# Kernel optimization log

Measured on AMD Instinct MI355X. Metric: run time of the kernel, lower is better.

Reference implementation:

```python
import jax, jax.numpy as jnp
import numpy as np

N_NODES = 50000
N_EDGES = 600000
F_IN = 128
HID = 128
N_CLASSES = 10


def _gcn_graph(edge_index, n_nodes):
    # PyG GCNConv: add self-loops, deg computed on target (col) with weight 1,
    # norm_e = deg^-1/2[src] * deg^-1/2[dst]
    src = jnp.concatenate([edge_index[0], jnp.arange(n_nodes, dtype=edge_index.dtype)])
    dst = jnp.concatenate([edge_index[1], jnp.arange(n_nodes, dtype=edge_index.dtype)])
    deg = jax.ops.segment_sum(jnp.ones_like(dst, dtype=jnp.float32), dst, num_segments=n_nodes)
    dinv = jnp.where(deg > 0, jax.lax.rsqrt(deg), 0.0)
    norm = dinv[src] * dinv[dst]  # [E+N]
    return src, dst, norm


def _gcn_layer(x, W, b, src, dst, norm, n_nodes):
    h = x @ W                      # [N, out] linear first (bias applied post-agg)
    m = h[src] * norm[:, None]     # gather + scale, [E+N, out]
    out = jax.ops.segment_sum(m, dst, num_segments=n_nodes)  # scatter-add
    return out + b


def setup_inputs() -> dict:
    key = jax.random.key(0)
    ks = jax.random.split(key, 4)
    x = jax.random.normal(ks[0], (N_NODES, F_IN), dtype=jnp.float32)
    edge_index = jax.random.randint(ks[1], (2, N_EDGES), 0, N_NODES, dtype=jnp.int64)
    # Glorot-ish init scale for weights
    W_stack = jax.random.normal(ks[2], (8, HID, HID), dtype=jnp.float32) * (1.0 / np.sqrt(HID))
    b_stack = jnp.zeros((8, HID), dtype=jnp.float32)
    W_out = jax.random.normal(ks[3], (HID, N_CLASSES), dtype=jnp.float32) * (1.0 / np.sqrt(HID))
    b_out = jnp.zeros((N_CLASSES,), dtype=jnp.float32)
    return {"x": x, "edge_index": edge_index, "W_stack": W_stack, "b_stack": b_stack,
            "W_out": W_out, "b_out": b_out}


def reference(x, edge_index, W_stack, b_stack, W_out, b_out):
    n_nodes = x.shape[0]
    src, dst, norm = _gcn_graph(edge_index, n_nodes)
    h = x
    for i in range(8):  # conv1..conv8 with ELU
        h = jax.nn.elu(_gcn_layer(h, W_stack[i], b_stack[i], src, dst, norm, n_nodes))
    # conv9: no activation
    return _gcn_layer(h, W_out, b_out, src, dst, norm, n_nodes)
```

## Files before the change

kernel.cpp:

```cpp
#include <hip/hip_runtime.h>
#include <math.h>

#define NN 50000
#define NE 600000
#define HID 128
#define NCLS 10
#define T2S 16

typedef __bf16 bf16x8 __attribute__((ext_vector_type(8)));
typedef float f32x16 __attribute__((ext_vector_type(16)));

__device__ __forceinline__ void split3(float f, ushort& h, ushort& m, ushort& l) {
    unsigned uh = __float_as_uint(f) & 0xffff0000u;
    float fm = f - __uint_as_float(uh);
    unsigned um = __float_as_uint(fm) & 0xffff0000u;
    float fl = fm - __uint_as_float(um);
    h = (ushort)(uh >> 16);
    m = (ushort)(um >> 16);
    l = (ushort)(__float_as_uint(fl) >> 16);
}


__global__ __launch_bounds__(256) void k_count(const int* __restrict__ edge,
                                               int* __restrict__ counts) {
    int e = blockIdx.x * 256 + threadIdx.x;
    if (e < NE) atomicAdd(&counts[edge[NE + e]], 1);
}

__device__ __forceinline__ int wave_incl_scan(int x, int lane) {
#pragma unroll
    for (int off = 1; off < 64; off <<= 1) {
        int y = __shfl_up(x, off, 64);
        if (lane >= off) x += y;
    }
    return x;
}

__global__ __launch_bounds__(256) void k_scan1(const int* __restrict__ counts,
                                               int* __restrict__ rowptr,
                                               int* __restrict__ bsum,
                                               float* __restrict__ dinv) {
    __shared__ int ws[4];
    int tid = threadIdx.x;
    int i = blockIdx.x * 256 + tid;
    int lane = tid & 63, wv = tid >> 6;
    int v = (i < NN) ? counts[i] : 0;
    if (i < NN) dinv[i] = rsqrtf((float)(v + 1));
    int x = wave_incl_scan(v, lane);
    if (lane == 63) ws[wv] = x;
    __syncthreads();
    int off = 0;
    for (int j = 0; j < wv; ++j) off += ws[j];
    if (i < NN) rowptr[i] = off + x - v;
    if (tid == 255) bsum[blockIdx.x] = off + x;
}

__global__ __launch_bounds__(256) void k_scan2(int* __restrict__ bsum, int n) {
    __shared__ int ws[4];
    int tid = threadIdx.x;
    int lane = tid & 63, wv = tid >> 6;
    int v = (tid < n) ? bsum[tid] : 0;
    int x = wave_incl_scan(v, lane);
    if (lane == 63) ws[wv] = x;
    __syncthreads();
    int off = 0;
    for (int j = 0; j < wv; ++j) off += ws[j];
    __syncthreads();
    if (tid < n) bsum[tid] = off + x - v;
}

__global__ __launch_bounds__(256) void k_scan3(int* __restrict__ rowptr,
                                               const int* __restrict__ bsum) {
    int i = blockIdx.x * 256 + threadIdx.x;
    if (i < NN) rowptr[i] += bsum[blockIdx.x];
    if (i == 0) rowptr[NN] = NE;
}

__global__ __launch_bounds__(256) void k_fill(const int* __restrict__ edge,
                                              const int* __restrict__ rowptr,
                                              int* __restrict__ cursor,
                                              const float* __restrict__ dinv,
                                              int2* __restrict__ csr) {
    int e = blockIdx.x * 256 + threadIdx.x;
    if (e >= NE) return;
    int s = edge[e], d = edge[NE + e];
    int slot = atomicSub(&cursor[d], 1) - 1;
    csr[rowptr[d] + slot] = make_int2(s, __float_as_int(dinv[s] * dinv[d]));
}


__global__ __launch_bounds__(256) void k_split_w(const float* __restrict__ Wst,
                                                 ushort* __restrict__ Wt4) {
    int i = blockIdx.x * 256 + threadIdx.x;
    if (i >= 8 * HID * HID) return;
    int l = i >> 14;
    int k = (i >> 7) & 127;
    int n = i & 127;
    ushort h, m, lo;
    split3(Wst[i], h, m, lo);
    int ks = k >> 4, r = k & 15;
    size_t base = ((((size_t)l * 3) * 8 + ks) * 128 + n) * 16 + r;
    const size_t pstride = (size_t)8 * 128 * 16;
    Wt4[base] = h;
    Wt4[base + pstride] = m;
    Wt4[base + 2 * pstride] = lo;
}


__global__ __launch_bounds__(256) void k_mfma_gemm(const float* __restrict__ H,
                                                   const ushort* __restrict__ Wt,
                                                   float* __restrict__ T) {
    int tid = threadIdx.x;
    int lane = tid & 63, w = tid >> 6;
    int l31 = lane & 31, lh = lane >> 5;
    int rowbase = blockIdx.x * 128;

    int grow = rowbase + w * 32 + l31;
    if (grow >= NN) grow = NN - 1;
    const float* arow = H + (size_t)grow * HID + lh * 8;

    const ushort* wbase = Wt + (size_t)l31 * 16 + lh * 8;

    f32x16 acc[4] = {};

#pragma unroll 2
    for (int s = 0; s < 8; ++s) {
        const float4* ap = (const float4*)(arow + s * 16);
        float4 f0 = ap[0], f1 = ap[1];
        float av[8] = {f0.x, f0.y, f0.z, f0.w, f1.x, f1.y, f1.z, f1.w};
        union { ushort u[8]; bf16x8 v; } ah, am, al;
#pragma unroll
        for (int q = 0; q < 8; ++q) split3(av[q], ah.u[q], am.u[q], al.u[q]);

        uint4 bf[3][4];
#pragma unroll
        for (int p = 0; p < 3; ++p)
#pragma unroll
            for (int c = 0; c < 4; ++c)
                bf[p][c] = *(const uint4*)(wbase + (((size_t)p * 8 + s) * 128 + c * 32) * 16);

#pragma unroll
        for (int c = 0; c < 4; ++c)
            acc[c] = __builtin_amdgcn_mfma_f32_32x32x16_bf16(ah.v, *(const bf16x8*)&bf[0][c], acc[c], 0, 0, 0);
#pragma unroll
        for (int c = 0; c < 4; ++c)
            acc[c] = __builtin_amdgcn_mfma_f32_32x32x16_bf16(ah.v, *(const bf16x8*)&bf[1][c], acc[c], 0, 0, 0);
#pragma unroll
        for (int c = 0; c < 4; ++c)
            acc[c] = __builtin_amdgcn_mfma_f32_32x32x16_bf16(am.v, *(const bf16x8*)&bf[0][c], acc[c], 0, 0, 0);
#pragma unroll
        for (int c = 0; c < 4; ++c)
            acc[c] = __builtin_amdgcn_mfma_f32_32x32x16_bf16(ah.v, *(const bf16x8*)&bf[2][c], acc[c], 0, 0, 0);
#pragma unroll
        for (int c = 0; c < 4; ++c)
            acc[c] = __builtin_amdgcn_mfma_f32_32x32x16_bf16(am.v, *(const bf16x8*)&bf[1][c], acc[c], 0, 0, 0);
#pragma unroll
        for (int c = 0; c < 4; ++c)
            acc[c] = __builtin_amdgcn_mfma_f32_32x32x16_bf16(al.v, *(const bf16x8*)&bf[0][c], acc[c], 0, 0, 0);
    }

#pragma unroll
    for (int c = 0; c < 4; ++c)
#pragma unroll
        for (int reg = 0; reg < 16; ++reg) {
            int r = (reg & 3) + 8 * (reg >> 2) + 4 * lh;
            int gr = rowbase + w * 32 + r;
            if (gr < NN)
                T[(size_t)gr * HID + c * 32 + l31] = acc[c][reg];
        }
}


__global__ __launch_bounds__(256) void k_gather_agg(const float* __restrict__ T,
                                                    float* __restrict__ Hout,
                                                    const int* __restrict__ rowptr,
                                                    const int2* __restrict__ csr,
                                                    const float* __restrict__ dinv,
                                                    const float* __restrict__ bias) {
    int lane = threadIdx.x & 63;
    int node = (blockIdx.x * 256 + threadIdx.x) >> 6;
    if (node >= NN) return;
    int slot = lane >> 5, l31 = lane & 31;

    int beg = rowptr[node], end = rowptr[node + 1];
    float sn = dinv[node];

    float4 acc = {0.f, 0.f, 0.f, 0.f};
    if (slot == 1) {
        float4 tv = ((const float4*)(T + (size_t)node * HID))[l31];
        float4 bv = ((const float4*)bias)[l31];
        float s2 = sn * sn;
        acc.x = s2 * tv.x + bv.x;
        acc.y = s2 * tv.y + bv.y;
        acc.z = s2 * tv.z + bv.z;
        acc.w = s2 * tv.w + bv.w;
    }

    const int2 zed = make_int2(0, 0);
    int p = beg + slot;
    int2 e0 = (p < end) ? csr[p] : zed;
    int2 e1 = (p + 2 < end) ? csr[p + 2] : zed;
    int2 e2 = (p + 4 < end) ? csr[p + 4] : zed;
    int2 e3 = (p + 6 < end) ? csr[p + 6] : zed;
    for (; p < end; p += 8) {
        float4 u0 = ((const float4*)(T + (size_t)e0.x * HID))[l31];
        float4 u1 = ((const float4*)(T + (size_t)e1.x * HID))[l31];
        float4 u2 = ((const float4*)(T + (size_t)e2.x * HID))[l31];
        float4 u3 = ((const float4*)(T + (size_t)e3.x * HID))[l31];
        float w0 = __int_as_float(e0.y), w1 = __int_as_float(e1.y);
        float w2 = __int_as_float(e2.y), w3 = __int_as_float(e3.y);
        e0 = (p + 8 < end) ? csr[p + 8] : zed;
        e1 = (p + 10 < end) ? csr[p + 10] : zed;
        e2 = (p + 12 < end) ? csr[p + 12] : zed;
        e3 = (p + 14 < end) ? csr[p + 14] : zed;
        acc.x += w0 * u0.x; acc.y += w0 * u0.y; acc.z += w0 * u0.z; acc.w += w0 * u0.w;
        acc.x += w1 * u1.x; acc.y += w1 * u1.y; acc.z += w1 * u1.z; acc.w += w1 * u1.w;
        acc.x += w2 * u2.x; acc.y += w2 * u2.y; acc.z += w2 * u2.z; acc.w += w2 * u2.w;
        acc.x += w3 * u3.x; acc.y += w3 * u3.y; acc.z += w3 * u3.z; acc.w += w3 * u3.w;
    }

    acc.x += __shfl_xor(acc.x, 32, 64);
    acc.y += __shfl_xor(acc.y, 32, 64);
    acc.z += __shfl_xor(acc.z, 32, 64);
    acc.w += __shfl_xor(acc.w, 32, 64);

    if (slot == 0) {
        float4 r = acc;
        r.x = r.x > 0.f ? r.x : expm1f(r.x);
        r.y = r.y > 0.f ? r.y : expm1f(r.y);
        r.z = r.z > 0.f ? r.z : expm1f(r.z);
        r.w = r.w > 0.f ? r.w : expm1f(r.w);
        ((float4*)(Hout + (size_t)node * HID))[l31] = r;
    }
}


__global__ __launch_bounds__(256) void k_matmul_out(const float* __restrict__ H,
                                                    const float* __restrict__ W,
                                                    float* __restrict__ T2) {
    __shared__ float Ws[128 * 11];
    int tid = threadIdx.x;
    for (int m = tid; m < HID * NCLS; m += 256) {
        int k = m / NCLS, c = m - k * NCLS;
        Ws[k * 11 + c] = W[m];
    }
    __syncthreads();
    int row = (blockIdx.x * 256 + tid) >> 4;
    int c16 = tid & 15;
    if (row >= NN) return;
    const float4* h4 = (const float4*)(H + (size_t)row * HID) + c16 * 2;
    float4 h0 = h4[0], h1 = h4[1];
    float hv[8] = {h0.x, h0.y, h0.z, h0.w, h1.x, h1.y, h1.z, h1.w};
    float acc[NCLS];
#pragma unroll
    for (int c = 0; c < NCLS; ++c) acc[c] = 0.f;
#pragma unroll
    for (int j = 0; j < 8; ++j) {
        const float* wr = &Ws[(c16 * 8 + j) * 11];
#pragma unroll
        for (int c = 0; c < NCLS; ++c) acc[c] += hv[j] * wr[c];
    }
#pragma unroll
    for (int off = 8; off >= 1; off >>= 1) {
#pragma unroll
        for (int c = 0; c < NCLS; ++c) acc[c] += __shfl_xor(acc[c], off, 16);
    }
    if (c16 < NCLS) T2[(size_t)row * T2S + c16] = acc[c16];
}

__global__ __launch_bounds__(256) void k_gather_out(const float* __restrict__ T2,
                                                    float* __restrict__ out,
                                                    const int* __restrict__ rowptr,
                                                    const int2* __restrict__ csr,
                                                    const float* __restrict__ dinv,
                                                    const float* __restrict__ bias) {
    int lane = threadIdx.x & 63;
    int node = (blockIdx.x * 256 + threadIdx.x) >> 6;
    if (node >= NN) return;
    int slot = lane >> 4, c = lane & 15;
    int beg = rowptr[node], end = rowptr[node + 1];
    float acc = 0.f;
    if (c < NCLS) {
        for (int i = beg + slot; i < end; i += 4) {
            int2 e = csr[i];
            acc += __int_as_float(e.y) * T2[(size_t)e.x * T2S + c];
        }
    }
    acc += __shfl_xor(acc, 16, 64);
    acc += __shfl_xor(acc, 32, 64);
    if (slot == 0 && c < NCLS) {
        float sn = dinv[node];
        sn *= sn;
        out[node * NCLS + c] = acc + sn * T2[(size_t)node * T2S + c] + bias[c];
    }
}


extern "C" void kernel_launch(void* const* d_in, const int* in_sizes, int n_in,
                              void* d_out, int out_size, void* d_ws, size_t ws_size,
                              hipStream_t stream) {
    (void)in_sizes; (void)n_in; (void)out_size; (void)ws_size;
    const float* x       = (const float*)d_in[0];
    const int*   edge    = (const int*)d_in[1];
    const float* W_stack = (const float*)d_in[2];
    const float* b_stack = (const float*)d_in[3];
    const float* W_out   = (const float*)d_in[4];
    const float* b_out   = (const float*)d_in[5];
    float* out = (float*)d_out;

    char* ws = (char*)d_ws;
    const size_t bigbuf = (size_t)NN * HID * sizeof(float);
    float* X      = (float*)ws;
    float* Y      = (float*)(ws + bigbuf);
    char*  p      = ws + 2 * bigbuf;
    int2*  csr    = (int2*)p;              p += sizeof(int2) * NE;
    float* dinv   = (float*)p;             p += sizeof(float) * NN;
    int*   rowptr = (int*)p;               p += sizeof(int) * (NN + 1);
    int*   counts = (int*)p;               p += sizeof(int) * NN;
    int*   bsum   = (int*)p;               p += sizeof(int) * 256;
    p = (char*)(((size_t)p + 15) & ~(size_t)15);
    ushort* Wt4 = (ushort*)p;  p += sizeof(ushort) * 8 * 3 * HID * HID;

    const int NB_N  = (NN + 255) / 256;
    const int NB_E  = (NE + 255) / 256;
    const int NB_G  = (NN + 127) / 128;
    const int NB_A  = (NN * 64 + 255) / 256;
    const int NB_W  = (NN * 64 + 255) / 256;
    const int NB_O  = (NN * 16 + 255) / 256;
    const int NB_SW = (8 * HID * HID + 255) / 256;

    hipMemsetAsync(counts, 0, sizeof(int) * NN, stream);
    k_count<<<NB_E, 256, 0, stream>>>(edge, counts);
    k_scan1<<<NB_N, 256, 0, stream>>>(counts, rowptr, bsum, dinv);
    k_scan2<<<1, 256, 0, stream>>>(bsum, NB_N);
    k_scan3<<<NB_N, 256, 0, stream>>>(rowptr, bsum);
    k_fill<<<NB_E, 256, 0, stream>>>(edge, rowptr, counts, dinv, csr);

    k_split_w<<<NB_SW, 256, 0, stream>>>(W_stack, Wt4);

    const float* Hin = x;
    for (int l = 0; l < 8; ++l) {
        k_mfma_gemm<<<NB_G, 256, 0, stream>>>(Hin, Wt4 + (size_t)l * 3 * HID * HID, Y);
        k_gather_agg<<<NB_A, 256, 0, stream>>>(Y, X, rowptr, csr, dinv,
                                               b_stack + (size_t)l * HID);
        Hin = X;
    }

    k_matmul_out<<<NB_O, 256, 0, stream>>>(X, W_out, Y);
    k_gather_out<<<NB_W, 256, 0, stream>>>(Y, out, rowptr, csr, dinv, b_out);
}
```

Baseline: 724.6 us.

## Fuse GCN aggregation with next layer's MFMA GEMM via shared memory

Adds a fused kernel that gathers and aggregates neighbour rows for 128 nodes, applies bias and ELU, stages the result in swizzled LDS, and then runs the next layer's split-bf16 MFMA GEMM directly from LDS. The point is to skip writing and re-reading the intermediate activation matrix between the aggregation and GEMM kernels, and to launch fewer kernels. The cost is that each block uses 64KB of LDS, which limits occupancy. Each 64-lane wave also now loops serially over 16 nodes, which may leave less parallelism to hide gather latency. The output layer now writes to a separate small buffer.

```diff
diff --git a/kernel.cpp b/kernel.cpp
--- a/kernel.cpp
+++ b/kernel.cpp
@@ -118,7 +118,6 @@
     int grow = rowbase + w * 32 + l31;
     if (grow >= NN) grow = NN - 1;
     const float* arow = H + (size_t)grow * HID + lh * 8;
-
     const ushort* wbase = Wt + (size_t)l31 * 16 + lh * 8;
 
     f32x16 acc[4] = {};
@@ -167,6 +166,136 @@
             int gr = rowbase + w * 32 + r;
             if (gr < NN)
                 T[(size_t)gr * HID + c * 32 + l31] = acc[c][reg];
+        }
+}
+
+
+__global__ __launch_bounds__(512, 4) void k_fused(const float* __restrict__ Tin,
+                                                  const ushort* __restrict__ Wt,
+                                                  const int* __restrict__ rowptr,
+                                                  const int2* __restrict__ csr,
+                                                  const float* __restrict__ dinv,
+                                                  const float* __restrict__ bias,
+                                                  float* __restrict__ Tout) {
+    __shared__ float Hs[128 * 128];
+    int tid = threadIdx.x;
+    int lane = tid & 63, w = tid >> 6;
+    int slot = lane >> 5, l31 = lane & 31;
+    int rowbase = blockIdx.x * 128;
+
+    float4 bv = ((const float4*)bias)[l31];
+
+    for (int i = 0; i < 16; ++i) {
+        int lrow = w * 16 + i;
+        int node = rowbase + lrow;
+        if (node >= NN) node = NN - 1;
+        int beg = rowptr[node], end = rowptr[node + 1];
+        float sn = dinv[node];
+
+        float4 acc = {0.f, 0.f, 0.f, 0.f};
+        if (slot == 1) {
+            float4 tv = ((const float4*)(Tin + (size_t)node * HID))[l31];
+            float s2 = sn * sn;
+            acc.x = s2 * tv.x + bv.x;
+            acc.y = s2 * tv.y + bv.y;
+            acc.z = s2 * tv.z + bv.z;
+            acc.w = s2 * tv.w + bv.w;
+        }
+
+        const int2 zed = make_int2(0, 0);
+        int p = beg + slot;
+        int2 e0 = (p < end) ? csr[p] : zed;
+        int2 e1 = (p + 2 < end) ? csr[p + 2] : zed;
+        int2 e2 = (p + 4 < end) ? csr[p + 4] : zed;
+        int2 e3 = (p + 6 < end) ? csr[p + 6] : zed;
+        for (; p < end; p += 8) {
+            float4 u0 = ((const float4*)(Tin + (size_t)e0.x * HID))[l31];
+            float4 u1 = ((const float4*)(Tin + (size_t)e1.x * HID))[l31];
+            float4 u2 = ((const float4*)(Tin + (size_t)e2.x * HID))[l31];
+            float4 u3 = ((const float4*)(Tin + (size_t)e3.x * HID))[l31];
+            float w0 = __int_as_float(e0.y), w1 = __int_as_float(e1.y);
+            float w2 = __int_as_float(e2.y), w3 = __int_as_float(e3.y);
+            e0 = (p + 8 < end) ? csr[p + 8] : zed;
+            e1 = (p + 10 < end) ? csr[p + 10] : zed;
+            e2 = (p + 12 < end) ? csr[p + 12] : zed;
+            e3 = (p + 14 < end) ? csr[p + 14] : zed;
+            acc.x += w0 * u0.x; acc.y += w0 * u0.y; acc.z += w0 * u0.z; acc.w += w0 * u0.w;
+            acc.x += w1 * u1.x; acc.y += w1 * u1.y; acc.z += w1 * u1.z; acc.w += w1 * u1.w;
+            acc.x += w2 * u2.x; acc.y += w2 * u2.y; acc.z += w2 * u2.z; acc.w += w2 * u2.w;
+            acc.x += w3 * u3.x; acc.y += w3 * u3.y; acc.z += w3 * u3.z; acc.w += w3 * u3.w;
+        }
+
+        acc.x += __shfl_xor(acc.x, 32, 64);
+        acc.y += __shfl_xor(acc.y, 32, 64);
+        acc.z += __shfl_xor(acc.z, 32, 64);
+        acc.w += __shfl_xor(acc.w, 32, 64);
+
+        if (slot == 0) {
+            float4 r = acc;
+            r.x = r.x > 0.f ? r.x : expm1f(r.x);
+            r.y = r.y > 0.f ? r.y : expm1f(r.y);
+            r.z = r.z > 0.f ? r.z : expm1f(r.z);
+            r.w = r.w > 0.f ? r.w : expm1f(r.w);
+            int byte = lrow * 512 + l31 * 16;
+            byte ^= (lrow & 7) << 4;
+            *(float4*)((char*)Hs + byte) = r;
+        }
+    }
+    __syncthreads();
+
+    int lh = slot;
+    int rloc = (w >> 1) * 32 + l31;
+    int colh = w & 1;
+    const ushort* wbase = Wt + ((size_t)(colh * 64) + l31) * 16 + lh * 8;
+
+    f32x16 acc2[2] = {};
+
+#pragma unroll 2
+    for (int s = 0; s < 8; ++s) {
+        int byte = rloc * 512 + s * 64 + lh * 32;
+        int sw = (rloc & 7) << 4;
+        float4 f0 = *(const float4*)((const char*)Hs + (byte ^ sw));
+        float4 f1 = *(const float4*)((const char*)Hs + ((byte + 16) ^ sw));
+        float av[8] = {f0.x, f0.y, f0.z, f0.w, f1.x, f1.y, f1.z, f1.w};
+        union { ushort u[8]; bf16x8 v; } ah, am, al;
+#pragma unroll
+        for (int q = 0; q < 8; ++q) split3(av[q], ah.u[q], am.u[q], al.u[q]);
+
+        uint4 bf[3][2];
+#pragma unroll
+        for (int p = 0; p < 3; ++p)
+#pragma unroll
+            for (int c = 0; c < 2; ++c)
+                bf[p][c] = *(const uint4*)(wbase + (((size_t)p * 8 + s) * 128 + c * 32) * 16);
+
+#pragma unroll
+        for (int c = 0; c < 2; ++c)
+            acc2[c] = __builtin_amdgcn_mfma_f32_32x32x16_bf16(ah.v, *(const bf16x8*)&bf[0][c], acc2[c], 0, 0, 0);
+#pragma unroll
+        for (int c = 0; c < 2; ++c)
+            acc2[c] = __builtin_amdgcn_mfma_f32_32x32x16_bf16(ah.v, *(const bf16x8*)&bf[1][c], acc2[c], 0, 0, 0);
+#pragma unroll
+        for (int c = 0; c < 2; ++c)
+            acc2[c] = __builtin_amdgcn_mfma_f32_32x32x16_bf16(am.v, *(const bf16x8*)&bf[0][c], acc2[c], 0, 0, 0);
+#pragma unroll
+        for (int c = 0; c < 2; ++c)
+            acc2[c] = __builtin_amdgcn_mfma_f32_32x32x16_bf16(ah.v, *(const bf16x8*)&bf[2][c], acc2[c], 0, 0, 0);
+#pragma unroll
+        for (int c = 0; c < 2; ++c)
+            acc2[c] = __builtin_amdgcn_mfma_f32_32x32x16_bf16(am.v, *(const bf16x8*)&bf[1][c], acc2[c], 0, 0, 0);
+#pragma unroll
+        for (int c = 0; c < 2; ++c)
+            acc2[c] = __builtin_amdgcn_mfma_f32_32x32x16_bf16(al.v, *(const bf16x8*)&bf[0][c], acc2[c], 0, 0, 0);
+    }
+
+#pragma unroll
+    for (int c = 0; c < 2; ++c)
+#pragma unroll
+        for (int reg = 0; reg < 16; ++reg) {
+            int r = (reg & 3) + 8 * (reg >> 2) + 4 * lh;
+            int gr = rowbase + (w >> 1) * 32 + r;
+            if (gr < NN)
+                Tout[(size_t)gr * HID + colh * 64 + c * 32 + l31] = acc2[c][reg];
         }
 }
 
@@ -320,12 +449,12 @@
     int*   bsum   = (int*)p;               p += sizeof(int) * 256;
     p = (char*)(((size_t)p + 15) & ~(size_t)15);
     ushort* Wt4 = (ushort*)p;  p += sizeof(ushort) * 8 * 3 * HID * HID;
+    float* T2b  = (float*)p;   p += sizeof(float) * NN * T2S;
 
     const int NB_N  = (NN + 255) / 256;
     const int NB_E  = (NE + 255) / 256;
     const int NB_G  = (NN + 127) / 128;
     const int NB_A  = (NN * 64 + 255) / 256;
-    const int NB_W  = (NN * 64 + 255) / 256;
     const int NB_O  = (NN * 16 + 255) / 256;
     const int NB_SW = (8 * HID * HID + 255) / 256;
 
@@ -338,14 +467,20 @@
 
     k_split_w<<<NB_SW, 256, 0, stream>>>(W_stack, Wt4);
 
-    const float* Hin = x;
-    for (int l = 0; l < 8; ++l) {
-        k_mfma_gemm<<<NB_G, 256, 0, stream>>>(Hin, Wt4 + (size_t)l * 3 * HID * HID, Y);
-        k_gather_agg<<<NB_A, 256, 0, stream>>>(Y, X, rowptr, csr, dinv,
-                                               b_stack + (size_t)l * HID);
-        Hin = X;
-    }
-
-    k_matmul_out<<<NB_O, 256, 0, stream>>>(X, W_out, Y);
-    k_gather_out<<<NB_W, 256, 0, stream>>>(Y, out, rowptr, csr, dinv, b_out);
-}
+    k_mfma_gemm<<<NB_G, 256, 0, stream>>>(x, Wt4, Y);
+
+    float* cur = Y;
+    float* nxt = X;
+    for (int l = 0; l < 7; ++l) {
+        k_fused<<<NB_G, 512, 0, stream>>>(cur, Wt4 + (size_t)(l + 1) * 3 * HID * HID,
+                                          rowptr, csr, dinv,
+                                          b_stack + (size_t)l * HID, nxt);
+        float* t = cur; cur = nxt; nxt = t;
+    }
+
+    k_gather_agg<<<NB_A, 256, 0, stream>>>(cur, nxt, rowptr, csr, dinv,
+                                           b_stack + (size_t)7 * HID);
+
+    k_matmul_out<<<NB_O, 256, 0, stream>>>(nxt, W_out, T2b);
+    k_gather_out<<<NB_A, 256, 0, stream>>>(T2b, out, rowptr, csr, dinv, b_out);
+}
```

New measurement: 685.4 us. -5.4%, faster.

## Fuse neighbor aggregation with next layer's MFMA GEMM through LDS

Applied to the files above, without the earlier changes.

Each layer's gather-aggregate and ELU now writes its 64-row tile into swizzled LDS, and the next layer's weight GEMM runs from LDS in the same kernel. This removes the global write and reread of the intermediate hidden activations and cuts the kernel launch count. The final aggregation is likewise fused with the small output matmul. In exchange, the gather runs with 8 nodes per wave serially, blocks are 512 threads with a 32KB LDS tile, and each wave now does a single 32x32 output tile, which may lower occupancy and gather latency hiding.

```diff
diff --git a/kernel.cpp b/kernel.cpp
--- a/kernel.cpp
+++ b/kernel.cpp
@@ -118,7 +118,6 @@
     int grow = rowbase + w * 32 + l31;
     if (grow >= NN) grow = NN - 1;
     const float* arow = H + (size_t)grow * HID + lh * 8;
-
     const ushort* wbase = Wt + (size_t)l31 * 16 + lh * 8;
 
     f32x16 acc[4] = {};
@@ -170,102 +169,182 @@
         }
 }
 
-
-__global__ __launch_bounds__(256) void k_gather_agg(const float* __restrict__ T,
-                                                    float* __restrict__ Hout,
-                                                    const int* __restrict__ rowptr,
-                                                    const int2* __restrict__ csr,
-                                                    const float* __restrict__ dinv,
-                                                    const float* __restrict__ bias) {
-    int lane = threadIdx.x & 63;
-    int node = (blockIdx.x * 256 + threadIdx.x) >> 6;
-    if (node >= NN) return;
+__device__ __forceinline__ void gather_to_lds(const float* __restrict__ Tin,
+                                              const int* __restrict__ rowptr,
+                                              const int2* __restrict__ csr,
+                                              const float* __restrict__ dinv,
+                                              float4 bv, float* Hs,
+                                              int rowbase, int w, int slot, int l31,
+                                              int nodes_per_wave) {
+    for (int i = 0; i < nodes_per_wave; ++i) {
+        int lrow = w * nodes_per_wave + i;
+        int node = rowbase + lrow;
+        if (node >= NN) node = NN - 1;
+        int beg = rowptr[node], end = rowptr[node + 1];
+        float sn = dinv[node];
+
+        float4 acc = {0.f, 0.f, 0.f, 0.f};
+        if (slot == 1) {
+            float4 tv = ((const float4*)(Tin + (size_t)node * HID))[l31];
+            float s2 = sn * sn;
+            acc.x = s2 * tv.x + bv.x;
+            acc.y = s2 * tv.y + bv.y;
+            acc.z = s2 * tv.z + bv.z;
+            acc.w = s2 * tv.w + bv.w;
+        }
+
+        const int2 zed = make_int2(0, 0);
+        int p = beg + slot;
+        int2 e0 = (p < end) ? csr[p] : zed;
+        int2 e1 = (p + 2 < end) ? csr[p + 2] : zed;
+        int2 e2 = (p + 4 < end) ? csr[p + 4] : zed;
+        int2 e3 = (p + 6 < end) ? csr[p + 6] : zed;
+        for (; p < end; p += 8) {
+            float4 u0 = ((const float4*)(Tin + (size_t)e0.x * HID))[l31];
+            float4 u1 = ((const float4*)(Tin + (size_t)e1.x * HID))[l31];
+            float4 u2 = ((const float4*)(Tin + (size_t)e2.x * HID))[l31];
+            float4 u3 = ((const float4*)(Tin + (size_t)e3.x * HID))[l31];
+            float w0 = __int_as_float(e0.y), w1 = __int_as_float(e1.y);
+            float w2 = __int_as_float(e2.y), w3 = __int_as_float(e3.y);
+            e0 = (p + 8 < end) ? csr[p + 8] : zed;
+            e1 = (p + 10 < end) ? csr[p + 10] : zed;
+            e2 = (p + 12 < end) ? csr[p + 12] : zed;
+            e3 = (p + 14 < end) ? csr[p + 14] : zed;
+            acc.x += w0 * u0.x; acc.y += w0 * u0.y; acc.z += w0 * u0.z; acc.w += w0 * u0.w;
+            acc.x += w1 * u1.x; acc.y += w1 * u1.y; acc.z += w1 * u1.z; acc.w += w1 * u1.w;
+            acc.x += w2 * u2.x; acc.y += w2 * u2.y; acc.z += w2 * u2.z; acc.w += w2 * u2.w;
+            acc.x += w3 * u3.x; acc.y += w3 * u3.y; acc.z += w3 * u3.z; acc.w += w3 * u3.w;
+        }
+
+        acc.x += __shfl_xor(acc.x, 32, 64);
+        acc.y += __shfl_xor(acc.y, 32, 64);
+        acc.z += __shfl_xor(acc.z, 32, 64);
+        acc.w += __shfl_xor(acc.w, 32, 64);
+
+        if (slot == 0) {
+            float4 r = acc;
+            r.x = r.x > 0.f ? r.x : expm1f(r.x);
+            r.y = r.y > 0.f ? r.y : expm1f(r.y);
+            r.z = r.z > 0.f ? r.z : expm1f(r.z);
+            r.w = r.w > 0.f ? r.w : expm1f(r.w);
+            int byte = lrow * 512 + l31 * 16;
+            byte ^= (lrow & 7) << 4;
+            *(float4*)((char*)Hs + byte) = r;
+        }
+    }
+}
+
+
+__global__ __launch_bounds__(512) void k_fused(const float* __restrict__ Tin,
+                                               const ushort* __restrict__ Wt,
+                                               const int* __restrict__ rowptr,
+                                               const int2* __restrict__ csr,
+                                               const float* __restrict__ dinv,
+                                               const float* __restrict__ bias,
+                                               float* __restrict__ Tout) {
+    __shared__ float Hs[64 * 128];
+    int tid = threadIdx.x;
+    int lane = tid & 63, w = tid >> 6;
     int slot = lane >> 5, l31 = lane & 31;
-
-    int beg = rowptr[node], end = rowptr[node + 1];
-    float sn = dinv[node];
-
-    float4 acc = {0.f, 0.f, 0.f, 0.f};
-    if (slot == 1) {
-        float4 tv = ((const float4*)(T + (size_t)node * HID))[l31];
-        float4 bv = ((const float4*)bias)[l31];
-        float s2 = sn * sn;
-        acc.x = s2 * tv.x + bv.x;
-        acc.y = s2 * tv.y + bv.y;
-        acc.z = s2 * tv.z + bv.z;
-        acc.w = s2 * tv.w + bv.w;
-    }
-
-    const int2 zed = make_int2(0, 0);
-    int p = beg + slot;
-    int2 e0 = (p < end) ? csr[p] : zed;
-    int2 e1 = (p + 2 < end) ? csr[p + 2] : zed;
-    int2 e2 = (p + 4 < end) ? csr[p + 4] : zed;
-    int2 e3 = (p + 6 < end) ? csr[p + 6] : zed;
-    for (; p < end; p += 8) {
-        float4 u0 = ((const float4*)(T + (size_t)e0.x * HID))[l31];
-        float4 u1 = ((const float4*)(T + (size_t)e1.x * HID))[l31];
-        float4 u2 = ((const float4*)(T + (size_t)e2.x * HID))[l31];
-        float4 u3 = ((const float4*)(T + (size_t)e3.x * HID))[l31];
-        float w0 = __int_as_float(e0.y), w1 = __int_as_float(e1.y);
-        float w2 = __int_as_float(e2.y), w3 = __int_as_float(e3.y);
-        e0 = (p + 8 < end) ? csr[p + 8] : zed;
-        e1 = (p + 10 < end) ? csr[p + 10] : zed;
-        e2 = (p + 12 < end) ? csr[p + 12] : zed;
-        e3 = (p + 14 < end) ? csr[p + 14] : zed;
-        acc.x += w0 * u0.x; acc.y += w0 * u0.y; acc.z += w0 * u0.z; acc.w += w0 * u0.w;
-        acc.x += w1 * u1.x; acc.y += w1 * u1.y; acc.z += w1 * u1.z; acc.w += w1 * u1.w;
-        acc.x += w2 * u2.x; acc.y += w2 * u2.y; acc.z += w2 * u2.z; acc.w += w2 * u2.w;
-        acc.x += w3 * u3.x; acc.y += w3 * u3.y; acc.z += w3 * u3.z; acc.w += w3 * u3.w;
-    }
-
-    acc.x += __shfl_xor(acc.x, 32, 64);
-    acc.y += __shfl_xor(acc.y, 32, 64);
-    acc.z += __shfl_xor(acc.z, 32, 64);
-    acc.w += __shfl_xor(acc.w, 32, 64);
-
-    if (slot == 0) {
-        float4 r = acc;
-        r.x = r.x > 0.f ? r.x : expm1f(r.x);
-        r.y = r.y > 0.f ? r.y : expm1f(r.y);
-        r.z = r.z > 0.f ? r.z : expm1f(r.z);
-        r.w = r.w > 0.f ? r.w : expm1f(r.w);
-        ((float4*)(Hout + (size_t)node * HID))[l31] = r;
-    }
-}
-
-
-__global__ __launch_bounds__(256) void k_matmul_out(const float* __restrict__ H,
-                                                    const float* __restrict__ W,
-                                                    float* __restrict__ T2) {
+    int rowbase = blockIdx.x * 64;
+
+    float4 bv = ((const float4*)bias)[l31];
+
+    gather_to_lds(Tin, rowptr, csr, dinv, bv, Hs, rowbase, w, slot, l31, 8);
+    __syncthreads();
+
+    int lh = slot;
+    int rloc = (w >> 2) * 32 + l31;
+    int colb = w & 3;
+    const ushort* wbase = Wt + ((size_t)(colb * 32) + l31) * 16 + lh * 8;
+
+    f32x16 acc2 = {};
+
+#pragma unroll 2
+    for (int s = 0; s < 8; ++s) {
+        int byte = rloc * 512 + s * 64 + lh * 32;
+        int sw = (rloc & 7) << 4;
+        float4 f0 = *(const float4*)((const char*)Hs + (byte ^ sw));
+        float4 f1 = *(const float4*)((const char*)Hs + ((byte + 16) ^ sw));
+        float av[8] = {f0.x, f0.y, f0.z, f0.w, f1.x, f1.y, f1.z, f1.w};
+        union { ushort u[8]; bf16x8 v; } ah, am, al;
+#pragma unroll
+        for (int q = 0; q < 8; ++q) split3(av[q], ah.u[q], am.u[q], al.u[q]);
+
+        uint4 bf[3];
+#pragma unroll
+        for (int p = 0; p < 3; ++p)
+            bf[p] = *(const uint4*)(wbase + (((size_t)p * 8 + s) * 128) * 16);
+
+        acc2 = __builtin_amdgcn_mfma_f32_32x32x16_bf16(ah.v, *(const bf16x8*)&bf[0], acc2, 0, 0, 0);
+        acc2 = __builtin_amdgcn_mfma_f32_32x32x16_bf16(ah.v, *(const bf16x8*)&bf[1], acc2, 0, 0, 0);
+        acc2 = __builtin_amdgcn_mfma_f32_32x32x16_bf16(am.v, *(const bf16x8*)&bf[0], acc2, 0, 0, 0);
+        acc2 = __builtin_amdgcn_mfma_f32_32x32x16_bf16(ah.v, *(const bf16x8*)&bf[2], acc2, 0, 0, 0);
+        acc2 = __builtin_amdgcn_mfma_f32_32x32x16_bf16(am.v, *(const bf16x8*)&bf[1], acc2, 0, 0, 0);
+        acc2 = __builtin_amdgcn_mfma_f32_32x32x16_bf16(al.v, *(const bf16x8*)&bf[0], acc2, 0, 0, 0);
+    }
+
+#pragma unroll
+    for (int reg = 0; reg < 16; ++reg) {
+        int r = (reg & 3) + 8 * (reg >> 2) + 4 * lh;
+        int gr = rowbase + (w >> 2) * 32 + r;
+        if (gr < NN)
+            Tout[(size_t)gr * HID + colb * 32 + l31] = acc2[reg];
+    }
+}
+
+
+__global__ __launch_bounds__(512) void k_fused_out(const float* __restrict__ Tin,
+                                                   const float* __restrict__ W,
+                                                   const int* __restrict__ rowptr,
+                                                   const int2* __restrict__ csr,
+                                                   const float* __restrict__ dinv,
+                                                   const float* __restrict__ bias,
+                                                   float* __restrict__ T2) {
+    __shared__ float Hs[64 * 128];
     __shared__ float Ws[128 * 11];
     int tid = threadIdx.x;
-    for (int m = tid; m < HID * NCLS; m += 256) {
+    int lane = tid & 63, w = tid >> 6;
+    int slot = lane >> 5, l31 = lane & 31;
+    int rowbase = blockIdx.x * 64;
+
+    for (int m = tid; m < HID * NCLS; m += 512) {
         int k = m / NCLS, c = m - k * NCLS;
         Ws[k * 11 + c] = W[m];
     }
+
+    float4 bv = ((const float4*)bias)[l31];
+    gather_to_lds(Tin, rowptr, csr, dinv, bv, Hs, rowbase, w, slot, l31, 8);
     __syncthreads();
-    int row = (blockIdx.x * 256 + tid) >> 4;
-    int c16 = tid & 15;
-    if (row >= NN) return;
-    const float4* h4 = (const float4*)(H + (size_t)row * HID) + c16 * 2;
-    float4 h0 = h4[0], h1 = h4[1];
-    float hv[8] = {h0.x, h0.y, h0.z, h0.w, h1.x, h1.y, h1.z, h1.w};
+
+    int row = tid >> 3;
+    int t8 = tid & 7;
     float acc[NCLS];
 #pragma unroll
     for (int c = 0; c < NCLS; ++c) acc[c] = 0.f;
-#pragma unroll
-    for (int j = 0; j < 8; ++j) {
-        const float* wr = &Ws[(c16 * 8 + j) * 11];
-#pragma unroll
-        for (int c = 0; c < NCLS; ++c) acc[c] += hv[j] * wr[c];
-    }
-#pragma unroll
-    for (int off = 8; off >= 1; off >>= 1) {
-#pragma unroll
-        for (int c = 0; c < NCLS; ++c) acc[c] += __shfl_xor(acc[c], off, 16);
-    }
-    if (c16 < NCLS) T2[(size_t)row * T2S + c16] = acc[c16];
+    int sw = (row & 7) << 4;
+    int base = row * 512 + t8 * 64;
+#pragma unroll
+    for (int q = 0; q < 4; ++q) {
+        float4 f = *(const float4*)((const char*)Hs + ((base + q * 16) ^ sw));
+        float hv[4] = {f.x, f.y, f.z, f.w};
+#pragma unroll
+        for (int j = 0; j < 4; ++j) {
+            const float* wr = &Ws[(t8 * 16 + q * 4 + j) * 11];
+#pragma unroll
+            for (int c = 0; c < NCLS; ++c) acc[c] += hv[j] * wr[c];
+        }
+    }
+#pragma unroll
+    for (int off = 4; off >= 1; off >>= 1) {
+#pragma unroll
+        for (int c = 0; c < NCLS; ++c) acc[c] += __shfl_xor(acc[c], off, 8);
+    }
+    int gr = rowbase + row;
+    if (t8 == 0 && gr < NN) {
+#pragma unroll
+        for (int c = 0; c < NCLS; ++c) T2[(size_t)gr * T2S + c] = acc[c];
+    }
 }
 
 __global__ __launch_bounds__(256) void k_gather_out(const float* __restrict__ T2,
@@ -320,13 +399,13 @@
     int*   bsum   = (int*)p;               p += sizeof(int) * 256;
     p = (char*)(((size_t)p + 15) & ~(size_t)15);
     ushort* Wt4 = (ushort*)p;  p += sizeof(ushort) * 8 * 3 * HID * HID;
+    float* T2b  = (float*)p;   p += sizeof(float) * NN * T2S;
 
     const int NB_N  = (NN + 255) / 256;
     const int NB_E  = (NE + 255) / 256;
     const int NB_G  = (NN + 127) / 128;
+    const int NB_F  = (NN + 63) / 64;
     const int NB_A  = (NN * 64 + 255) / 256;
-    const int NB_W  = (NN * 64 + 255) / 256;
-    const int NB_O  = (NN * 16 + 255) / 256;
     const int NB_SW = (8 * HID * HID + 255) / 256;
 
     hipMemsetAsync(counts, 0, sizeof(int) * NN, stream);
@@ -338,14 +417,19 @@
 
     k_split_w<<<NB_SW, 256, 0, stream>>>(W_stack, Wt4);
 
-    const float* Hin = x;
-    for (int l = 0; l < 8; ++l) {
-        k_mfma_gemm<<<NB_G, 256, 0, stream>>>(Hin, Wt4 + (size_t)l * 3 * HID * HID, Y);
-        k_gather_agg<<<NB_A, 256, 0, stream>>>(Y, X, rowptr, csr, dinv,
-                                               b_stack + (size_t)l * HID);
-        Hin = X;
-    }
-
-    k_matmul_out<<<NB_O, 256, 0, stream>>>(X, W_out, Y);
-    k_gather_out<<<NB_W, 256, 0, stream>>>(Y, out, rowptr, csr, dinv, b_out);
-}
+    k_mfma_gemm<<<NB_G, 256, 0, stream>>>(x, Wt4, Y);
+
+    float* cur = Y;
+    float* nxt = X;
+    for (int l = 0; l < 7; ++l) {
+        k_fused<<<NB_F, 512, 0, stream>>>(cur, Wt4 + (size_t)(l + 1) * 3 * HID * HID,
+                                          rowptr, csr, dinv,
+                                          b_stack + (size_t)l * HID, nxt);
+        float* t = cur; cur = nxt; nxt = t;
+    }
+
+    k_fused_out<<<NB_F, 512, 0, stream>>>(cur, W_out, rowptr, csr, dinv,
+                                          b_stack + (size_t)7 * HID, T2b);
+
+    k_gather_out<<<NB_A, 256, 0, stream>>>(T2b, out, rowptr, csr, dinv, b_out);
+}
```

Measured after the change: 733.2 us. No clear change (+1.2%).
